# Kernel optimization log

Hardware: AMD Instinct MI355X
Metric: run time of the kernel (lower is better)

The kernel has to match this reference:

```python
import jax, jax.numpy as jnp
import numpy as np

N = 100000        # nodes
E = 1600000       # edges (avg degree 16)
H = 128           # hidden dim
LAYERS = 3
RESIDUAL = 1.0


def setup_inputs() -> dict:
    key = jax.random.key(0)
    ks = jax.random.split(key, 7)
    x = jax.random.normal(ks[0], (N, H), dtype=jnp.float32)
    src = jax.random.randint(ks[1], (E,), 0, N, dtype=jnp.int32)
    dst = jax.random.randint(ks[2], (E,), 0, N, dtype=jnp.int32)
    s = 1.0 / np.sqrt(H)
    W1 = jax.random.normal(ks[3], (H, H), dtype=jnp.float32) * s
    b1 = jnp.zeros((H,), dtype=jnp.float32)
    W2 = jax.random.normal(ks[4], (H, H), dtype=jnp.float32) * s
    b2 = jnp.zeros((H,), dtype=jnp.float32)
    return {"x": x, "src": src, "dst": dst, "W1": W1, "b1": b1, "W2": W2, "b2": b2}


def _gcn_conv(h, src, dst, dinv, W, b):
    # PyG GCNConv: h' = D^{-1/2}(A+I)D^{-1/2} (h W) + b
    h = h @ W                                   # [N,H]
    norm = dinv[src] * dinv[dst]                # [E]
    msgs = h[src] * norm[:, None]               # [E,H] gather (memory-bound)
    agg = jax.ops.segment_sum(msgs, dst, num_segments=N)  # scatter-add
    agg = agg + h * (dinv * dinv)[:, None]      # self-loop contribution
    return agg + b


def reference(x, src, dst, W1, b1, W2, b2):
    # symmetric degree normalization with self-loops (deg over dst, + 1 for self-loop)
    deg = jax.ops.segment_sum(jnp.ones((E,), x.dtype), dst, num_segments=N) + 1.0
    dinv = jax.lax.rsqrt(deg)                   # [N]

    ori = x
    h = _gcn_conv(x, src, dst, dinv, W1, b1) + RESIDUAL * ori
    for _ in range(LAYERS - 1):
        h = jax.nn.relu(h)                      # dropout is identity in eval mode
        h = _gcn_conv(h, src, dst, dinv, W2, b2) + RESIDUAL * ori
    return h
```

## Files before the change

kernel.cpp:

```cpp
#include <hip/hip_runtime.h>

#define H 128
#define AP 136
#define BSH 9
#define BSZ 512
#define MAXB 256
#define NBLK 256

typedef __attribute__((ext_vector_type(8))) short short8;
typedef __attribute__((ext_vector_type(4))) float floatx4;
typedef __attribute__((ext_vector_type(2))) float f32x2;

__device__ inline unsigned short f2b(float f) {
  union { float f; unsigned u; } v; v.f = f;
  unsigned r = v.u + 0x7fffu + ((v.u >> 16) & 1u);
  return (unsigned short)(r >> 16);
}
__device__ inline float blo(unsigned u) { return __uint_as_float(u << 16); }
__device__ inline float bhi(unsigned u) { return __uint_as_float(u & 0xffff0000u); }
__device__ inline unsigned char f2f8(float f) {
  return (unsigned char)(__builtin_amdgcn_cvt_pk_fp8_f32(f, f, 0, false) & 0xff);
}
__device__ inline f32x2 fp8x2(unsigned u) {
#if __has_builtin(__builtin_amdgcn_cvt_pk_f32_fp8)
  return __builtin_amdgcn_cvt_pk_f32_fp8(u, false);
#else
  f32x2 r;
  r.x = __builtin_amdgcn_cvt_f32_fp8(u, 0);
  r.y = __builtin_amdgcn_cvt_f32_fp8(u, 1);
  return r;
#endif
}


__global__ __launch_bounds__(256) void k_bh_prep(const int* __restrict__ dst,
                                                 int* __restrict__ bhist,
                                                 int E, int NB, int chunk,
                                                 const float* __restrict__ W1,
                                                 const float* __restrict__ W2,
                                                 unsigned short* __restrict__ Wt1,
                                                 unsigned short* __restrict__ Wt2,
                                                 const float* __restrict__ x,
                                                 unsigned int* __restrict__ xb,
                                                 int xtotal) {
  int tid = threadIdx.x;
  int bx = blockIdx.x;
  if (bx < NBLK) {
    __shared__ int hst[MAXB];
    hst[tid] = 0;
    __syncthreads();
    int s = bx * chunk;
    int eend = min(s + chunk, E);
    for (int e = s + tid; e < eend; e += 256)
      atomicAdd(&hst[dst[e] >> BSH], 1);
    __syncthreads();
    if (tid < NB) bhist[tid * NBLK + bx] = hst[tid];
  } else if (bx < NBLK + 2) {
    const float* W = (bx - NBLK) ? W2 : W1;
    unsigned short* Wt = (bx - NBLK) ? Wt2 : Wt1;
#pragma unroll
    for (int i = 0; i < 64; i++) {
      int idx = tid + 256 * i;
      int k = idx >> 7, n = idx & 127;
      Wt[n * 128 + k] = f2b(W[idx]);
    }
  } else {
    int i = (bx - NBLK - 2) * 256 + tid;
    if (i < xtotal) {
      float2 v = ((const float2*)x)[i];
      xb[i] = (unsigned)f2b(v.x) | ((unsigned)f2b(v.y) << 16);
    }
  }
}

__global__ __launch_bounds__(512) void k_bscan(const int* __restrict__ bhist,
                                               int* __restrict__ boff2, int total) {
  __shared__ int ps[512];
  int tid = threadIdx.x;
  int base = tid * 128;
  int4 v[32];
  int sum = 0;
  if (base < total) {
    const int4* row = (const int4*)(bhist + base);
#pragma unroll
    for (int j = 0; j < 32; j++) v[j] = row[j];
#pragma unroll
    for (int j = 0; j < 32; j++) sum += v[j].x + v[j].y + v[j].z + v[j].w;
  }
  ps[tid] = sum;
  __syncthreads();
  for (int off = 1; off < 512; off <<= 1) {
    int t = (tid >= off) ? ps[tid - off] : 0;
    __syncthreads();
    ps[tid] += t;
    __syncthreads();
  }
  int run = ps[tid] - sum;
  if (base < total) {
    int4* orow = (int4*)(boff2 + base);
#pragma unroll
    for (int j = 0; j < 32; j++) {
      int4 o;
      o.x = run; run += v[j].x;
      o.y = run; run += v[j].y;
      o.z = run; run += v[j].z;
      o.w = run; run += v[j].w;
      orow[j] = o;
    }
  }
}

__global__ __launch_bounds__(256) void k_bscatter(const int* __restrict__ src,
                                                  const int* __restrict__ dst,
                                                  const int* __restrict__ boff2,
                                                  int* __restrict__ bed,
                                                  int E, int NB, int chunk) {
  __shared__ int pos[MAXB];
  int tid = threadIdx.x;
  if (tid < NB) pos[tid] = boff2[tid * NBLK + blockIdx.x];
  __syncthreads();
  int s = blockIdx.x * chunk;
  int eend = min(s + chunk, E);
  for (int e = s + tid; e < eend; e += 256) {
    int d = dst[e];
    int p = atomicAdd(&pos[d >> BSH], 1);
    bed[p] = (src[e] << BSH) | (d & (BSZ - 1));
  }
}

__global__ __launch_bounds__(512) void k_build(const int* __restrict__ bed,
                                               const int* __restrict__ boff2,
                                               int* __restrict__ roff,
                                               float* __restrict__ dinv,
                                               int* __restrict__ csr,
                                               int N, int E, int NB) {
  __shared__ int cnt[BSZ];
  __shared__ int pos[BSZ];
  __shared__ int ps[BSZ];
  int b = blockIdx.x, tid = threadIdx.x;
  int bs = boff2[b * NBLK];
  int be = (b + 1 < NB) ? boff2[(b + 1) * NBLK] : E;
  int n0 = b << BSH;
  cnt[tid] = 0;
  __syncthreads();
  for (int e = bs + tid; e < be; e += 512)
    atomicAdd(&cnt[bed[e] & (BSZ - 1)], 1);
  __syncthreads();
  int c = cnt[tid];
  ps[tid] = c;
  __syncthreads();
  for (int off = 1; off < 512; off <<= 1) {
    int t = (tid >= off) ? ps[tid - off] : 0;
    __syncthreads();
    ps[tid] += t;
    __syncthreads();
  }
  int base = bs + ps[tid] - c;
  pos[tid] = base;
  int node = n0 + tid;
  if (node < N) {
    roff[node] = base;
    dinv[node] = rsqrtf((float)c + 1.0f);
  }
  __syncthreads();
  for (int e = bs + tid; e < be; e += 512) {
    int v = bed[e];
    int p = atomicAdd(&pos[v & (BSZ - 1)], 1);
    csr[p] = v >> BSH;
  }
  if (b == 0 && tid == 0) roff[N] = E;
}

__global__ __launch_bounds__(256) void k_gemm(const unsigned int* __restrict__ in,
                                              const unsigned short* __restrict__ Wt,
                                              unsigned char* __restrict__ out,
                                              int n) {
  __shared__ short As[64 * AP];
  __shared__ short Bs[128 * AP];
  int tid = threadIdx.x;
  int wave = tid >> 6, lane = tid & 63;
  int quad = lane >> 4, l16 = lane & 15;
  int row0 = blockIdx.x * 64;

  const float4* in4 = (const float4*)in;
#pragma unroll
  for (int i = 0; i < 4; i++) {
    int idx = tid + 256 * i;
    int r = idx >> 4, c = idx & 15;
    int gr = row0 + r;
    float4 v = make_float4(0.f, 0.f, 0.f, 0.f);
    if (gr < n) v = in4[(size_t)gr * 16 + c];
    *(float4*)&As[r * AP + c * 8] = v;
  }
  const float4* Wt4 = (const float4*)Wt;
#pragma unroll
  for (int i = 0; i < 8; i++) {
    int idx = tid + 256 * i;
    int nr = idx >> 4, c = idx & 15;
    *(float4*)&Bs[nr * AP + c * 8] = Wt4[nr * 16 + c];
  }
  __syncthreads();

  floatx4 acc[4][2];
#pragma unroll
  for (int mt = 0; mt < 4; mt++)
#pragma unroll
    for (int nt = 0; nt < 2; nt++) acc[mt][nt] = (floatx4)(0.f);

#pragma unroll
  for (int ks = 0; ks < 4; ks++) {
    short8 a[4], b[2];
#pragma unroll
    for (int mt = 0; mt < 4; mt++)
      a[mt] = *(const short8*)&As[(mt * 16 + l16) * AP + ks * 32 + quad * 8];
#pragma unroll
    for (int nt = 0; nt < 2; nt++)
      b[nt] = *(const short8*)&Bs[(wave * 32 + nt * 16 + l16) * AP + ks * 32 + quad * 8];
#pragma unroll
    for (int mt = 0; mt < 4; mt++)
#pragma unroll
      for (int nt = 0; nt < 2; nt++)
        acc[mt][nt] = __builtin_amdgcn_mfma_f32_16x16x32_bf16(a[mt], b[nt], acc[mt][nt], 0, 0, 0);
  }

#pragma unroll
  for (int mt = 0; mt < 4; mt++) {
#pragma unroll
    for (int nt = 0; nt < 2; nt++) {
#pragma unroll
      for (int r = 0; r < 4; r++) {
        int gr = row0 + mt * 16 + quad * 4 + r;
        if (gr < n)
          out[(size_t)gr * H + wave * 32 + nt * 16 + l16] = f2f8(acc[mt][nt][r]);
      }
    }
  }
}

__global__ __launch_bounds__(256) void k_agg(const unsigned short* __restrict__ h,
                                             const int* __restrict__ csr,
                                             const int* __restrict__ roff,
                                             const float* __restrict__ dinv,
                                             const float* __restrict__ bias,
                                             const unsigned int* __restrict__ xb,
                                             float* __restrict__ out32,
                                             unsigned int* __restrict__ out16,
                                             int n, int write16) {
  int wave = threadIdx.x >> 6;
  int lane = threadIdx.x & 63;
  int node = blockIdx.x * 4 + wave;
  if (node >= n) return;

  float di = dinv[node];
  unsigned su = h[(size_t)node * 64 + lane];
  unsigned xu = xb[(size_t)node * 64 + lane];
  float2 bv = ((const float2*)bias)[lane];
  f32x2 sp = fp8x2(su);
  float acc0 = bv.x + blo(xu) + di * di * sp.x;
  float acc1 = bv.y + bhi(xu) + di * di * sp.y;

  int e0u = __builtin_amdgcn_readfirstlane(roff[node]);
  int e1u = __builtin_amdgcn_readfirstlane(roff[node + 1]);
  int last = e1u - 1;
  for (int e = e0u; e < e1u; e += 16) {
    int idx[16];
#pragma unroll
    for (int k = 0; k < 16; k++) {
      int ee = min(e + k, last);
      idx[k] = __builtin_amdgcn_readfirstlane(csr[ee]);
    }
    unsigned u[16];
#pragma unroll
    for (int k = 0; k < 16; k++) u[k] = (h + ((size_t)idx[k] << 6))[lane];
    float cf[16];
#pragma unroll
    for (int k = 0; k < 16; k++)
      cf[k] = (e + k <= last) ? di * dinv[idx[k]] : 0.f;
#pragma unroll
    for (int k = 0; k < 16; k++) {
      f32x2 p = fp8x2(u[k]);
      acc0 += cf[k] * p.x;
      acc1 += cf[k] * p.y;
    }
  }
  if (write16) {
    out16[(size_t)node * 64 + lane] =
        (unsigned)f2b(fmaxf(acc0, 0.f)) | ((unsigned)f2b(fmaxf(acc1, 0.f)) << 16);
  } else {
    ((float2*)out32)[(size_t)node * 64 + lane] = make_float2(acc0, acc1);
  }
}

extern "C" void kernel_launch(void* const* d_in, const int* in_sizes, int n_in,
                              void* d_out, int out_size, void* d_ws, size_t ws_size,
                              hipStream_t stream) {
  const float* x = (const float*)d_in[0];
  const int* src = (const int*)d_in[1];
  const int* dst = (const int*)d_in[2];
  const float* W1 = (const float*)d_in[3];
  const float* b1 = (const float*)d_in[4];
  const float* W2 = (const float*)d_in[5];
  const float* b2 = (const float*)d_in[6];
  int N = in_sizes[0] / H;
  int E = in_sizes[1];
  float* out = (float*)d_out;

  char* p = (char*)d_ws;
  auto alloc = [&](size_t bytes) {
    char* q = p;
    p += (bytes + 255) & ~(size_t)255;
    return q;
  };
  int* roff = (int*)alloc((size_t)(N + 1) * 4);
  float* dinv = (float*)alloc((size_t)N * 4);
  int* csr = (int*)alloc((size_t)E * 4);
  unsigned int* xb = (unsigned int*)alloc((size_t)N * H * 2);
  unsigned char* htmp = (unsigned char*)alloc((size_t)N * H);
  unsigned int* fbuf = (unsigned int*)alloc((size_t)N * H * 2);
  unsigned short* Wt1 = (unsigned short*)alloc(128 * 128 * 2);
  unsigned short* Wt2 = (unsigned short*)alloc(128 * 128 * 2);
  int* bhist = (int*)alloc((size_t)MAXB * NBLK * 4);
  int* boff2 = (int*)alloc((size_t)MAXB * NBLK * 4);
  int* bed = (int*)alloc((size_t)E * 4);

  int NB = (N + BSZ - 1) >> BSH;
  int chunk = (E + NBLK - 1) / NBLK;

  int xtotal = N * (H / 2);
  int xblocks = (xtotal + 255) / 256;

  k_bh_prep<<<NBLK + 2 + xblocks, 256, 0, stream>>>(dst, bhist, E, NB, chunk,
                                                    W1, W2, Wt1, Wt2, x, xb, xtotal);
  k_bscan<<<1, 512, 0, stream>>>(bhist, boff2, NB * NBLK);
  k_bscatter<<<NBLK, 256, 0, stream>>>(src, dst, boff2, bed, E, NB, chunk);
  k_build<<<NB, 512, 0, stream>>>(bed, boff2, roff, dinv, csr, N, E, NB);

  int gb = (N + 63) / 64;
  int ab = (N + 3) / 4;

  k_gemm<<<gb, 256, 0, stream>>>(xb, Wt1, htmp, N);
  k_agg<<<ab, 256, 0, stream>>>((const unsigned short*)htmp, csr, roff, dinv, b1, xb,
                                nullptr, fbuf, N, 1);
  k_gemm<<<gb, 256, 0, stream>>>(fbuf, Wt2, htmp, N);
  k_agg<<<ab, 256, 0, stream>>>((const unsigned short*)htmp, csr, roff, dinv, b2, xb,
                                nullptr, fbuf, N, 1);
  k_gemm<<<gb, 256, 0, stream>>>(fbuf, Wt2, htmp, N);
  k_agg<<<ab, 256, 0, stream>>>((const unsigned short*)htmp, csr, roff, dinv, b2, xb,
                                out, nullptr, N, 0);
}
```

Before: 444.3 us.

## Precompute per-edge dinv array and split agg loop into 16/4/1 tails

Adds extra blocks to the first GEMM launch that fill a per-edge array holding dinv[csr[e]]. Each aggregation layer then reads this array contiguously instead of gathering dinv through neighbor indices. The edge loop is also split into 16-wide, 4-wide and scalar parts, so the clamped padded gathers in the tail disappear. In exchange it costs an extra E-sized float buffer and one more pass over csr, and the scalar loads now come from two streams.

```diff
diff --git a/kernel.cpp b/kernel.cpp
--- a/kernel.cpp
+++ b/kernel.cpp
@@ -30,6 +30,11 @@
   r.y = __builtin_amdgcn_cvt_f32_fp8(u, 1);
   return r;
 #endif
+}
+__device__ inline float rfl_f(float x) {
+  union { float f; int i; } u; u.f = x;
+  u.i = __builtin_amdgcn_readfirstlane(u.i);
+  return u.f;
 }
 
 
@@ -174,7 +179,25 @@
 __global__ __launch_bounds__(256) void k_gemm(const unsigned int* __restrict__ in,
                                               const unsigned short* __restrict__ Wt,
                                               unsigned char* __restrict__ out,
-                                              int n) {
+                                              int n, int gb,
+                                              const int* __restrict__ csr,
+                                              const float* __restrict__ dinv,
+                                              float* __restrict__ cfa, int Ecf) {
+  if (blockIdx.x >= gb) {
+    int i0 = (blockIdx.x - gb) * 2048 + threadIdx.x * 8;
+    if (i0 + 8 <= Ecf) {
+      int4 c0 = *(const int4*)(csr + i0);
+      int4 c1 = *(const int4*)(csr + i0 + 4);
+      float4 f0, f1;
+      f0.x = dinv[c0.x]; f0.y = dinv[c0.y]; f0.z = dinv[c0.z]; f0.w = dinv[c0.w];
+      f1.x = dinv[c1.x]; f1.y = dinv[c1.y]; f1.z = dinv[c1.z]; f1.w = dinv[c1.w];
+      *(float4*)(cfa + i0) = f0;
+      *(float4*)(cfa + i0 + 4) = f1;
+    } else {
+      for (int i = i0; i < Ecf; i++) cfa[i] = dinv[csr[i]];
+    }
+    return;
+  }
   __shared__ short As[64 * AP];
   __shared__ short Bs[128 * AP];
   int tid = threadIdx.x;
@@ -241,6 +264,7 @@
                                              const int* __restrict__ csr,
                                              const int* __restrict__ roff,
                                              const float* __restrict__ dinv,
+                                             const float* __restrict__ cfa,
                                              const float* __restrict__ bias,
                                              const unsigned int* __restrict__ xb,
                                              float* __restrict__ out32,
@@ -259,29 +283,52 @@
   float acc0 = bv.x + blo(xu) + di * di * sp.x;
   float acc1 = bv.y + bhi(xu) + di * di * sp.y;
 
-  int e0u = __builtin_amdgcn_readfirstlane(roff[node]);
-  int e1u = __builtin_amdgcn_readfirstlane(roff[node + 1]);
-  int last = e1u - 1;
-  for (int e = e0u; e < e1u; e += 16) {
+  int e0 = roff[node], e1 = roff[node + 1];
+  int e = e0;
+  for (; e + 16 <= e1; e += 16) {
+    int eu = __builtin_amdgcn_readfirstlane(e);
+    float cf[16];
+#pragma unroll
+    for (int k = 0; k < 16; k++) cf[k] = di * rfl_f(cfa[eu + k]);
     int idx[16];
 #pragma unroll
-    for (int k = 0; k < 16; k++) {
-      int ee = min(e + k, last);
-      idx[k] = __builtin_amdgcn_readfirstlane(csr[ee]);
-    }
+    for (int k = 0; k < 16; k++) idx[k] = __builtin_amdgcn_readfirstlane(csr[eu + k]);
     unsigned u[16];
 #pragma unroll
     for (int k = 0; k < 16; k++) u[k] = (h + ((size_t)idx[k] << 6))[lane];
-    float cf[16];
-#pragma unroll
-    for (int k = 0; k < 16; k++)
-      cf[k] = (e + k <= last) ? di * dinv[idx[k]] : 0.f;
 #pragma unroll
     for (int k = 0; k < 16; k++) {
       f32x2 p = fp8x2(u[k]);
       acc0 += cf[k] * p.x;
       acc1 += cf[k] * p.y;
     }
+  }
+  for (; e + 4 <= e1; e += 4) {
+    int eu = __builtin_amdgcn_readfirstlane(e);
+    float cf[4];
+#pragma unroll
+    for (int k = 0; k < 4; k++) cf[k] = di * rfl_f(cfa[eu + k]);
+    int idx[4];
+#pragma unroll
+    for (int k = 0; k < 4; k++) idx[k] = __builtin_amdgcn_readfirstlane(csr[eu + k]);
+    unsigned u[4];
+#pragma unroll
+    for (int k = 0; k < 4; k++) u[k] = (h + ((size_t)idx[k] << 6))[lane];
+#pragma unroll
+    for (int k = 0; k < 4; k++) {
+      f32x2 p = fp8x2(u[k]);
+      acc0 += cf[k] * p.x;
+      acc1 += cf[k] * p.y;
+    }
+  }
+  for (; e < e1; e++) {
+    int eu = __builtin_amdgcn_readfirstlane(e);
+    float cf = di * rfl_f(cfa[eu]);
+    int s = __builtin_amdgcn_readfirstlane(csr[eu]);
+    unsigned u = h[(size_t)s * 64 + lane];
+    f32x2 p = fp8x2(u);
+    acc0 += cf * p.x;
+    acc1 += cf * p.y;
   }
   if (write16) {
     out16[(size_t)node * 64 + lane] =
@@ -314,6 +361,7 @@
   int* roff = (int*)alloc((size_t)(N + 1) * 4);
   float* dinv = (float*)alloc((size_t)N * 4);
   int* csr = (int*)alloc((size_t)E * 4);
+  float* cfa = (float*)alloc((size_t)E * 4);
   unsigned int* xb = (unsigned int*)alloc((size_t)N * H * 2);
   unsigned char* htmp = (unsigned char*)alloc((size_t)N * H);
   unsigned int* fbuf = (unsigned int*)alloc((size_t)N * H * 2);
@@ -337,14 +385,15 @@
 
   int gb = (N + 63) / 64;
   int ab = (N + 3) / 4;
-
-  k_gemm<<<gb, 256, 0, stream>>>(xb, Wt1, htmp, N);
-  k_agg<<<ab, 256, 0, stream>>>((const unsigned short*)htmp, csr, roff, dinv, b1, xb,
-                                nullptr, fbuf, N, 1);
-  k_gemm<<<gb, 256, 0, stream>>>(fbuf, Wt2, htmp, N);
-  k_agg<<<ab, 256, 0, stream>>>((const unsigned short*)htmp, csr, roff, dinv, b2, xb,
-                                nullptr, fbuf, N, 1);
-  k_gemm<<<gb, 256, 0, stream>>>(fbuf, Wt2, htmp, N);
-  k_agg<<<ab, 256, 0, stream>>>((const unsigned short*)htmp, csr, roff, dinv, b2, xb,
-                                out, nullptr, N, 0);
-}
+  int cfblocks = (E + 2047) / 2048;
+
+  k_gemm<<<gb + cfblocks, 256, 0, stream>>>(xb, Wt1, htmp, N, gb, csr, dinv, cfa, E);
+  k_agg<<<ab, 256, 0, stream>>>((const unsigned short*)htmp, csr, roff, dinv, cfa, b1,
+                                xb, nullptr, fbuf, N, 1);
+  k_gemm<<<gb, 256, 0, stream>>>(fbuf, Wt2, htmp, N, gb, nullptr, nullptr, nullptr, 0);
+  k_agg<<<ab, 256, 0, stream>>>((const unsigned short*)htmp, csr, roff, dinv, cfa, b2,
+                                xb, nullptr, fbuf, N, 1);
+  k_gemm<<<gb, 256, 0, stream>>>(fbuf, Wt2, htmp, N, gb, nullptr, nullptr, nullptr, 0);
+  k_agg<<<ab, 256, 0, stream>>>((const unsigned short*)htmp, csr, roff, dinv, cfa, b2,
+                                xb, out, nullptr, N, 0);
+}
```

Result: faster. 378.4 us (-14.8%).
